# Kernel tuning notes

Measured on AMD Instinct MI355X. Metric: run time of the kernel, lower is better.

The kernel has to match this reference:

```python
import jax, jax.numpy as jnp
import numpy as np
import math

N, C, H = 2048, 256, 8
D = C // H
T, R, E = 8, 12, 32768
BUCKETS = 21
SEED = 128


def _layernorm(x, g, b, eps=1e-5):
    mu = jnp.mean(x, axis=-1, keepdims=True)
    var = jnp.var(x, axis=-1, keepdims=True)
    return (x - mu) * jax.lax.rsqrt(var + eps) * g + b


def _bucketize_dt(dt, num_buckets):
    eps = 1e-06
    signed_log = jnp.sign(dt) * jnp.log1p(jnp.abs(dt) + eps)
    min_v, max_v = -5.0, 5.0
    norm = (jnp.clip(signed_log, min_v, max_v) - min_v) / (max_v - min_v + 1e-09)
    idx = jnp.floor(norm * (num_buckets - 1)).astype(jnp.int32)
    return jnp.clip(idx, 0, num_buckets - 1)


def setup_inputs() -> dict:
    key = jax.random.key(0)
    ks = jax.random.split(key, 24)
    s = 0.02
    inp = {
        'X': jax.random.normal(ks[0], (N, C), jnp.float32),
        'token_type': jax.random.randint(ks[1], (N,), 0, T, jnp.int32),
        'edge_src': jax.random.randint(ks[2], (E,), 0, N, jnp.int32),
        'edge_dst': jax.random.randint(ks[3], (E,), 0, N, jnp.int32),
        'edge_rel': jax.random.randint(ks[4], (E,), 0, R, jnp.int32),
        'time_vec': jax.random.normal(ks[5], (N,), jnp.float32),
        'seed_count': SEED,
        'Wq': jax.random.normal(ks[6], (C, C), jnp.float32) * s,
        'bq': jnp.zeros((C,), jnp.float32),
        'Wk': jax.random.normal(ks[7], (C, C), jnp.float32) * s,
        'bk': jnp.zeros((C,), jnp.float32),
        'Wv': jax.random.normal(ks[8], (C, C), jnp.float32) * s,
        'bv': jnp.zeros((C,), jnp.float32),
        'Wo': jax.random.normal(ks[9], (C, C), jnp.float32) * s,
        'bo': jnp.zeros((C,), jnp.float32),
        'ln1_g': jnp.ones((C,), jnp.float32),
        'ln1_b': jnp.zeros((C,), jnp.float32),
        'ln2_g': jnp.ones((C,), jnp.float32),
        'ln2_b': jnp.zeros((C,), jnp.float32),
        'W1': jax.random.normal(ks[10], (C, 4 * C), jnp.float32) * s,
        'b1': jnp.zeros((4 * C,), jnp.float32),
        'W2': jax.random.normal(ks[11], (4 * C, C), jnp.float32) * s,
        'b2': jnp.zeros((C,), jnp.float32),
        'adj_rel_bias': jnp.zeros((R, H), jnp.float32),
        'typepair_bias': jnp.zeros((T, T, H), jnp.float32),
        'temp_bias': jax.random.normal(ks[12], (BUCKETS, H), jnp.float32) * s,
    }
    return inp


def reference(X, token_type, edge_src, edge_dst, edge_rel, time_vec, seed_count,
              Wq, bq, Wk, bk, Wv, bv, Wo, bo,
              ln1_g, ln1_b, ln2_g, ln2_b, W1, b1, W2, b2,
              adj_rel_bias, typepair_bias, temp_bias):
    n = X.shape[0]
    h = _layernorm(X, ln1_g, ln1_b)
    q = (h @ Wq + bq).reshape(n, H, D)
    k = (h @ Wk + bk).reshape(n, H, D)
    v = (h @ Wv + bv).reshape(n, H, D)
    scores = jnp.einsum('nhd,mhd->hnm', q, k) / math.sqrt(D)  # [H, N, N]

    # structural bias, factored as [N, N, H] then transposed
    bias = typepair_bias[token_type][:, token_type]            # [N, N, H]
    bias = bias.at[edge_src, edge_dst].add(adj_rel_bias[edge_rel])
    # seed-wise temporal bias on the first seed_count rows
    dt = time_vec[None, :] - time_vec[:seed_count, None]       # [S, N]
    tb = temp_bias[_bucketize_dt(dt, BUCKETS)]                 # [S, N, H]
    bias = bias.at[:seed_count].add(tb)

    attn = jax.nn.softmax(scores + bias.transpose(2, 0, 1), axis=-1)
    o = jnp.einsum('hnm,mhd->nhd', attn, v).reshape(n, C)
    x = X + (o @ Wo + bo)

    h2 = _layernorm(x, ln2_g, ln2_b)
    f = jax.nn.gelu(h2 @ W1 + b1, approximate=False) @ W2 + b2
    return x + f
```

## Files before the change

### kernel.cpp

```cpp
#include <hip/hip_runtime.h>
#include <hip/hip_bf16.h>
#include <math.h>

#define NTOK 2048
#define CDIM 256
#define HHEADS 8
#define DHEAD 32
#define NEDGE 32768
#define NTILE2 32
#define EXTD 64
#define LE 72
#define LP2 136

typedef __attribute__((ext_vector_type(8))) short short8;
typedef __attribute__((ext_vector_type(4))) short short4v;
typedef __attribute__((ext_vector_type(4))) float f32x4;

static __device__ inline short f2bf(float f) {
    __hip_bfloat16 h = __float2bfloat16(f);
    return *reinterpret_cast<short*>(&h);
}
static __device__ inline float bf2f(short s) {
    unsigned int u = ((unsigned int)(unsigned short)s) << 16;
    return *reinterpret_cast<float*>(&u);
}

static __device__ inline void transpose_tile_f32(const float* __restrict__ in,
    short* __restrict__ out, int K, int N, int k0, int n0, int t)
{
    __shared__ float tile[64][65];
    int r0 = t >> 4, c0 = (t & 15) * 4;
    #pragma unroll
    for (int i = 0; i < 4; i++) {
        int r = r0 + i * 16;
        float4 v = *(const float4*)(in + (size_t)(k0 + r) * N + n0 + c0);
        tile[r][c0 + 0] = v.x; tile[r][c0 + 1] = v.y;
        tile[r][c0 + 2] = v.z; tile[r][c0 + 3] = v.w;
    }
    __syncthreads();
    #pragma unroll
    for (int i = 0; i < 4; i++) {
        int nr = r0 + i * 16;
        short o4[4];
        #pragma unroll
        for (int j = 0; j < 4; j++) o4[j] = f2bf(tile[c0 + j][nr]);
        *(short4v*)(out + (size_t)(n0 + nr) * K + k0 + c0) = *(short4v*)o4;
    }
}

__global__ __launch_bounds__(256) void prep_kernel(
    const float* __restrict__ Wq, const float* __restrict__ Wk,
    const float* __restrict__ Wv, const float* __restrict__ Wo,
    const float* __restrict__ W1, const float* __restrict__ W2,
    short* __restrict__ wt_qkv, short* __restrict__ wot,
    short* __restrict__ w1t, short* __restrict__ w2t,
    const int* __restrict__ token_type, const float* __restrict__ typepair_bias,
    short* __restrict__ qh, short* __restrict__ kh,
    int* __restrict__ cnt2, float* __restrict__ rowsum,
    const float* __restrict__ X, const float* __restrict__ ln1_g,
    const float* __restrict__ ln1_b, short* __restrict__ h1)
{
    int b = blockIdx.x;
    int t = threadIdx.x;
    if (b < 192) {
        const float* src; short* dst; int K, N, bx, by;
        if (b < 64) {
            int m = b >> 4, r = b & 15;
            src = (m == 0) ? Wq : (m == 1) ? Wk : (m == 2) ? Wv : Wo;
            dst = (m == 0) ? wt_qkv : (m == 1) ? wt_qkv + 256 * 256
                : (m == 2) ? wt_qkv + 512 * 256 : wot;
            K = 256; N = 256; bx = r & 3; by = r >> 2;
        } else if (b < 128) {
            int r = b - 64; src = W1; dst = w1t; K = 256; N = 1024; bx = r & 15; by = r >> 4;
        } else {
            int r = b - 128; src = W2; dst = w2t; K = 1024; N = 256; bx = r & 3; by = r >> 2;
        }
        transpose_tile_f32(src, dst, K, N, by * 64, bx * 64, t);
    } else if (b < 256) {
        int idx = (b - 192) * 256 + t;
        int row = idx >> 3, h = idx & 7;
        int tt = token_type[row];
        short qe[32], ke[32];
        #pragma unroll
        for (int j = 0; j < 32; j++) {
            if (j < 8) {
                qe[j] = f2bf(typepair_bias[(tt * 8 + j) * 8 + h]);
                ke[j] = (j == tt) ? (short)0x3F80 : (short)0;
            } else { qe[j] = 0; ke[j] = 0; }
        }
        size_t base = ((size_t)h * NTOK + row) * EXTD + 32;
        #pragma unroll
        for (int k = 0; k < 4; k++) {
            *(short8*)&qh[base + k * 8] = *(short8*)&qe[k * 8];
            *(short8*)&kh[base + k * 8] = *(short8*)&ke[k * 8];
        }
    } else if (b < 288) {
        int base = (b - 256) * 2048 + t * 8;
        #pragma unroll
        for (int i = 0; i < 8; i++) cnt2[base + i] = 0;
    } else if (b < 296) {
        int base = (b - 288) * 2048 + t * 8;
        #pragma unroll
        for (int i = 0; i < 8; i++) rowsum[base + i] = 0.0f;
    } else {
        int wv = t >> 6, lane = t & 63;
        int row = (b - 296) * 4 + wv;
        float4 x = *(const float4*)&X[(size_t)row * CDIM + lane * 4];
        float s = x.x + x.y + x.z + x.w;
        #pragma unroll
        for (int off = 1; off < 64; off <<= 1) s += __shfl_xor(s, off);
        float mu = s * (1.0f / CDIM);
        float4 d = { x.x - mu, x.y - mu, x.z - mu, x.w - mu };
        float s2 = d.x * d.x + d.y * d.y + d.z * d.z + d.w * d.w;
        #pragma unroll
        for (int off = 1; off < 64; off <<= 1) s2 += __shfl_xor(s2, off);
        float rsig = rsqrtf(s2 * (1.0f / CDIM) + 1e-5f);
        float4 gg = *(const float4*)&ln1_g[lane * 4];
        float4 bb = *(const float4*)&ln1_b[lane * 4];
        short o4[4];
        o4[0] = f2bf(d.x * rsig * gg.x + bb.x);
        o4[1] = f2bf(d.y * rsig * gg.y + bb.y);
        o4[2] = f2bf(d.z * rsig * gg.z + bb.z);
        o4[3] = f2bf(d.w * rsig * gg.w + bb.w);
        *(short4v*)&h1[(size_t)row * CDIM + lane * 4] = *(short4v*)o4;
    }
}

__global__ __launch_bounds__(256) void ln4_kernel(const float* __restrict__ X,
    const float* __restrict__ g, const float* __restrict__ b, short* __restrict__ out)
{
    int t = threadIdx.x;
    int wv = t >> 6, lane = t & 63;
    int row = blockIdx.x * 4 + wv;

    float4 x = *(const float4*)&X[(size_t)row * CDIM + lane * 4];
    float s = x.x + x.y + x.z + x.w;
    #pragma unroll
    for (int off = 1; off < 64; off <<= 1) s += __shfl_xor(s, off);
    float mu = s * (1.0f / CDIM);
    float4 d = { x.x - mu, x.y - mu, x.z - mu, x.w - mu };
    float s2 = d.x * d.x + d.y * d.y + d.z * d.z + d.w * d.w;
    #pragma unroll
    for (int off = 1; off < 64; off <<= 1) s2 += __shfl_xor(s2, off);
    float rsig = rsqrtf(s2 * (1.0f / CDIM) + 1e-5f);
    float4 gg = *(const float4*)&g[lane * 4];
    float4 bb = *(const float4*)&b[lane * 4];
    short o4[4];
    o4[0] = f2bf(d.x * rsig * gg.x + bb.x);
    o4[1] = f2bf(d.y * rsig * gg.y + bb.y);
    o4[2] = f2bf(d.z * rsig * gg.z + bb.z);
    o4[3] = f2bf(d.w * rsig * gg.w + bb.w);
    *(short4v*)&out[(size_t)row * CDIM + lane * 4] = *(short4v*)o4;
}

template<int EPI>
__global__ __launch_bounds__(256) void gemm32_kernel(
    const short* __restrict__ A, const short* __restrict__ Bt,
    const float* __restrict__ bias, const float* __restrict__ resid,
    void* __restrict__ out_, int M, int N, int K)
{
    __shared__ short A_lds[32 * 40];
    __shared__ short B_lds[64 * 40];

    const int t = threadIdx.x;
    const int w = t >> 6, lane = t & 63, c = lane & 15, g = lane >> 4;
    const int row0 = blockIdx.y * 32, col0 = blockIdx.x * 64;
    const int srow = t >> 2, sk = (t & 3) * 8;

    f32x4 acc[2] = {};

    for (int k0 = 0; k0 < K; k0 += 32) {
        if (t < 128)
            *(short8*)&A_lds[srow * 40 + sk] = *(const short8*)&A[(size_t)(row0 + srow) * K + k0 + sk];
        *(short8*)&B_lds[srow * 40 + sk] = *(const short8*)&Bt[(size_t)(col0 + srow) * K + k0 + sk];
        __syncthreads();
        short8 af = *(const short8*)&A_lds[((w & 1) * 16 + c) * 40 + g * 8];
        #pragma unroll
        for (int nf = 0; nf < 2; nf++) {
            short8 bf = *(const short8*)&B_lds[((w >> 1) * 32 + nf * 16 + c) * 40 + g * 8];
            acc[nf] = __builtin_amdgcn_mfma_f32_16x16x32_bf16(af, bf, acc[nf], 0, 0, 0);
        }
        __syncthreads();
    }

    #pragma unroll
    for (int nf = 0; nf < 2; nf++) {
        #pragma unroll
        for (int reg = 0; reg < 4; reg++) {
            int row = row0 + (w & 1) * 16 + g * 4 + reg;
            int col = col0 + (w >> 1) * 32 + nf * 16 + c;
            float v = acc[nf][reg] + bias[col];
            if (EPI == 2) {
                ((float*)out_)[(size_t)row * N + col] = v + resid[(size_t)row * N + col];
            } else {
                v = 0.5f * v * (1.0f + erff(v * 0.70710678118654752f));
                ((short*)out_)[(size_t)row * N + col] = f2bf(v);
            }
        }
    }
}

__global__ __launch_bounds__(256) void gemm32_qkv_kernel(
    const short* __restrict__ A, const short* __restrict__ Bt,
    const float* __restrict__ bq, const float* __restrict__ bk, const float* __restrict__ bv,
    short* __restrict__ qh, short* __restrict__ kh, short* __restrict__ vt)
{
    const int K = CDIM;
    __shared__ short A_lds[32 * 40];
    __shared__ short B_lds[64 * 40];

    const int t = threadIdx.x;
    const int w = t >> 6, lane = t & 63, c = lane & 15, g = lane >> 4;
    const int row0 = blockIdx.y * 32, col0 = blockIdx.x * 64;
    const int srow = t >> 2, sk = (t & 3) * 8;

    f32x4 acc[2] = {};

    for (int k0 = 0; k0 < K; k0 += 32) {
        if (t < 128)
            *(short8*)&A_lds[srow * 40 + sk] = *(const short8*)&A[(size_t)(row0 + srow) * K + k0 + sk];
        *(short8*)&B_lds[srow * 40 + sk] = *(const short8*)&Bt[(size_t)(col0 + srow) * K + k0 + sk];
        __syncthreads();
        short8 af = *(const short8*)&A_lds[((w & 1) * 16 + c) * 40 + g * 8];
        #pragma unroll
        for (int nf = 0; nf < 2; nf++) {
            short8 bf = *(const short8*)&B_lds[((w >> 1) * 32 + nf * 16 + c) * 40 + g * 8];
            acc[nf] = __builtin_amdgcn_mfma_f32_16x16x32_bf16(af, bf, acc[nf], 0, 0, 0);
        }
        __syncthreads();
    }

    const int region = col0 >> 8;
    const int colr0 = col0 & 255;
    const float* bias = (region == 0) ? bq : (region == 1) ? bk : bv;
    #pragma unroll
    for (int nf = 0; nf < 2; nf++) {
        #pragma unroll
        for (int reg = 0; reg < 4; reg++) {
            int row = row0 + (w & 1) * 16 + g * 4 + reg;
            int col = colr0 + (w >> 1) * 32 + nf * 16 + c;
            float v = acc[nf][reg] + bias[col];
            if (region == 0) v *= 0.17677669529663687f;
            short bb = f2bf(v);
            size_t hidx = ((size_t)(col >> 5) * NTOK + row) * EXTD + (col & 31);
            if (region == 0)      qh[hidx] = bb;
            else if (region == 1) kh[hidx] = bb;
            else {
                int rl = row & 63;
                int rp = ((rl & 15) << 2) | (rl >> 4);
                vt[(size_t)col * NTOK + (row & ~63) + rp] = bb;
            }
        }
    }
}

__global__ void edge_hist2_kernel(const int* __restrict__ src, const int* __restrict__ dst,
    int* __restrict__ cnt, int E)
{
    int e = blockIdx.x * blockDim.x + threadIdx.x;
    if (e < E) atomicAdd(&cnt[src[e] * NTILE2 + (dst[e] >> 6)], 1);
}

__global__ __launch_bounds__(256) void edge_scan2_kernel(const int* __restrict__ cnt,
    int* __restrict__ row_ptr, int* __restrict__ wcur)
{
    __shared__ int sums[256];
    int t = threadIdx.x;
    int base = t * 256;
    int s = 0;
    for (int i = 0; i < 64; i++) {
        int4 v = *(const int4*)&cnt[base + i * 4];
        s += v.x + v.y + v.z + v.w;
    }
    sums[t] = s;
    __syncthreads();
    for (int off = 1; off < 256; off <<= 1) {
        int v = (t >= off) ? sums[t - off] : 0;
        __syncthreads();
        sums[t] += v;
        __syncthreads();
    }
    int run = (t == 0) ? 0 : sums[t - 1];
    for (int i = 0; i < 64; i++) {
        int4 v = *(const int4*)&cnt[base + i * 4];
        int4 o;
        o.x = run; run += v.x;
        o.y = run; run += v.y;
        o.z = run; run += v.z;
        o.w = run; run += v.w;
        *(int4*)&row_ptr[base + i * 4] = o;
        *(int4*)&wcur[base + i * 4] = o;
    }
    if (t == 255) row_ptr[NTOK * NTILE2] = run;
}

__global__ void edge_scatter2_kernel(const int* __restrict__ src, const int* __restrict__ dst,
    const int* __restrict__ rel, int* __restrict__ wcur, int2* __restrict__ pairs, int E)
{
    int e = blockIdx.x * blockDim.x + threadIdx.x;
    if (e < E) {
        int d = dst[e];
        int pos = atomicAdd(&wcur[src[e] * NTILE2 + (d >> 6)], 1);
        pairs[pos] = make_int2(d, rel[e]);
    }
}

__global__ __launch_bounds__(256) void sgemm_exp_kernel(
    const short* __restrict__ qh, const short* __restrict__ kh,
    const float* __restrict__ time_vec, const int* __restrict__ seed_ptr,
    const float* __restrict__ adj_rel_bias, const float* __restrict__ temp_bias,
    const int* __restrict__ row_ptr2, const int2* __restrict__ pairs2,
    short* __restrict__ S, float* __restrict__ rowsum)
{
    __shared__ short A_lds[64 * LE];
    __shared__ short B_lds[64 * LE];
    __shared__ float tcol_s[64];
    __shared__ float temp_h[21];
    __shared__ float adj_h[12];
    __shared__ int rpA[64], rpB[64];

    const int t = threadIdx.x;
    const int w = t >> 6, lane = t & 63, c = lane & 15, g = lane >> 4;
    const int h = blockIdx.z;
    const int m0 = blockIdx.x * 64, n0 = blockIdx.y * 64;
    const int seed = seed_ptr[0];

    {
        int r = t >> 3, off = (t & 7) * 8;
        *(short8*)&A_lds[r * LE + off] =
            *(const short8*)&qh[((size_t)h * NTOK + n0 + r) * EXTD + off];
        *(short8*)&A_lds[(r + 32) * LE + off] =
            *(const short8*)&qh[((size_t)h * NTOK + n0 + 32 + r) * EXTD + off];
        *(short8*)&B_lds[r * LE + off] =
            *(const short8*)&kh[((size_t)h * NTOK + m0 + r) * EXTD + off];
        *(short8*)&B_lds[(r + 32) * LE + off] =
            *(const short8*)&kh[((size_t)h * NTOK + m0 + 32 + r) * EXTD + off];
    }
    if (t < 64) {
        tcol_s[t] = time_vec[m0 + t];
        int bidx = (n0 + t) * NTILE2 + (m0 >> 6);
        rpA[t] = row_ptr2[bidx];
        rpB[t] = row_ptr2[bidx + 1];
    }
    if (t < 21) temp_h[t] = temp_bias[t * HHEADS + h];
    if (t < 12) adj_h[t] = adj_rel_bias[t * HHEADS + h];
    __syncthreads();

    short8 alo = *(const short8*)&A_lds[(w * 16 + c) * LE + g * 8];
    short8 ahi = *(const short8*)&A_lds[(w * 16 + c) * LE + 32 + g * 8];
    f32x4 acc[4] = {};
    #pragma unroll
    for (int nf = 0; nf < 4; nf++) {
        short8 blo = *(const short8*)&B_lds[(nf * 16 + c) * LE + g * 8];
        short8 bhi = *(const short8*)&B_lds[(nf * 16 + c) * LE + 32 + g * 8];
        acc[nf] = __builtin_amdgcn_mfma_f32_16x16x32_bf16(alo, blo, acc[nf], 0, 0, 0);
        acc[nf] = __builtin_amdgcn_mfma_f32_16x16x32_bf16(ahi, bhi, acc[nf], 0, 0, 0);
    }

    #pragma unroll
    for (int reg = 0; reg < 4; reg++) {
        const int rloc = w * 16 + g * 4 + reg;
        const int n = n0 + rloc;
        const bool rowTemp = (n < seed);
        const float tn = rowTemp ? time_vec[n] : 0.0f;

        {
            int e0 = rpA[rloc], e1 = rpB[rloc];
            for (int e = e0; e < e1; ++e) {
                int2 pr = pairs2[e];
                int cl = pr.x & 63;
                if ((cl & 15) == c) {
                    float ab = adj_h[pr.y];
                    int nfi = cl >> 4;
                    #pragma unroll
                    for (int nf = 0; nf < 4; nf++)
                        if (nf == nfi) acc[nf][reg] += ab;
                }
            }
        }

        float rsum = 0.0f;
        short p4[4];
        #pragma unroll
        for (int nf = 0; nf < 4; nf++) {
            float s = acc[nf][reg];
            if (rowTemp) {
                float dt = tcol_s[nf * 16 + c] - tn;
                float ab = fabsf(dt) + 1e-6f;
                float sg = (dt > 0.0f) ? 1.0f : ((dt < 0.0f) ? -1.0f : 0.0f);
                float sl = sg * log1pf(ab);
                sl = fminf(fmaxf(sl, -5.0f), 5.0f);
                float norm = (sl + 5.0f) * (1.0f / (10.0f + 1e-9f));
                int bidx = (int)floorf(norm * 20.0f);
                bidx = min(max(bidx, 0), 20);
                s += temp_h[bidx];
            }
            float e = __expf(s);
            rsum += e;
            p4[nf] = f2bf(e);
        }
        *(short4v*)&S[((size_t)h * NTOK + n) * NTOK + m0 + c * 4] = *(short4v*)p4;
        rsum += __shfl_xor(rsum, 1);
        rsum += __shfl_xor(rsum, 2);
        rsum += __shfl_xor(rsum, 4);
        rsum += __shfl_xor(rsum, 8);
        if (c == 0) atomicAdd(&rowsum[h * NTOK + n], rsum);
    }
}

__global__ __launch_bounds__(256) void pv_kernel(
    const short* __restrict__ P, const short* __restrict__ vt,
    const float* __restrict__ rowsum, short* __restrict__ o)
{
    __shared__ short A_lds[32 * LP2];
    __shared__ short B_lds[32 * LP2];
    const int t = threadIdx.x;
    const int w = t >> 6, lane = t & 63, c = lane & 15, g = lane >> 4;
    const int h = blockIdx.y;
    const int n0 = blockIdx.x * 32;
    const int rowblk = (w & 1) * 16, colblk = (w >> 1) * 16;

    f32x4 acc = {0.0f, 0.0f, 0.0f, 0.0f};

    for (int k0 = 0; k0 < NTOK; k0 += 128) {
        #pragma unroll
        for (int i = 0; i < 2; i++) {
            int s = t + i * 256;
            int r = s >> 4, off = (s & 15) * 8;
            *(short8*)&A_lds[r * LP2 + off] =
                *(const short8*)&P[((size_t)h * NTOK + n0 + r) * NTOK + k0 + off];
            *(short8*)&B_lds[r * LP2 + off] =
                *(const short8*)&vt[(size_t)(h * 32 + r) * NTOK + k0 + off];
        }
        __syncthreads();
        #pragma unroll
        for (int kk = 0; kk < 4; kk++) {
            short8 af = *(const short8*)&A_lds[(rowblk + c) * LP2 + kk * 32 + g * 8];
            short8 bf = *(const short8*)&B_lds[(colblk + c) * LP2 + kk * 32 + g * 8];
            acc = __builtin_amdgcn_mfma_f32_16x16x32_bf16(af, bf, acc, 0, 0, 0);
        }
        __syncthreads();
    }

    #pragma unroll
    for (int reg = 0; reg < 4; reg++) {
        int row = n0 + rowblk + g * 4 + reg;
        int col = h * 32 + colblk + c;
        float inv = 1.0f / rowsum[h * NTOK + row];
        o[(size_t)row * CDIM + col] = f2bf(acc[reg] * inv);
    }
}

extern "C" void kernel_launch(void* const* d_in, const int* in_sizes, int n_in,
                              void* d_out, int out_size, void* d_ws, size_t ws_size,
                              hipStream_t stream)
{
    (void)in_sizes; (void)n_in; (void)out_size; (void)ws_size;
    const float* X        = (const float*)d_in[0];
    const int* token_type = (const int*)d_in[1];
    const int* edge_src   = (const int*)d_in[2];
    const int* edge_dst   = (const int*)d_in[3];
    const int* edge_rel   = (const int*)d_in[4];
    const float* time_vec = (const float*)d_in[5];
    const int* seed_ptr   = (const int*)d_in[6];
    const float* Wq = (const float*)d_in[7];  const float* bq = (const float*)d_in[8];
    const float* Wk = (const float*)d_in[9];  const float* bk = (const float*)d_in[10];
    const float* Wv = (const float*)d_in[11]; const float* bv = (const float*)d_in[12];
    const float* Wo = (const float*)d_in[13]; const float* bo = (const float*)d_in[14];
    const float* ln1_g = (const float*)d_in[15]; const float* ln1_b = (const float*)d_in[16];
    const float* ln2_g = (const float*)d_in[17]; const float* ln2_b = (const float*)d_in[18];
    const float* W1 = (const float*)d_in[19]; const float* b1 = (const float*)d_in[20];
    const float* W2 = (const float*)d_in[21]; const float* b2 = (const float*)d_in[22];
    const float* adj_rel_bias  = (const float*)d_in[23];
    const float* typepair_bias = (const float*)d_in[24];
    const float* temp_bias     = (const float*)d_in[25];
    float* out = (float*)d_out;

    char* base = (char*)d_ws;
    size_t off = 0;
    auto alloc = [&](size_t bytes) { char* p = base + off; off += (bytes + 255) & ~(size_t)255; return p; };
    short* qh_bf   = (short*)alloc((size_t)HHEADS * NTOK * EXTD * 2);
    short* kh_bf   = (short*)alloc((size_t)HHEADS * NTOK * EXTD * 2);
    short* vt_bf   = (short*)alloc((size_t)256 * NTOK * 2);
    short* h1_bf   = (short*)alloc((size_t)NTOK * 256 * 2);
    short* h2_bf   = (short*)alloc((size_t)NTOK * 256 * 2);
    short* o_bf    = (short*)alloc((size_t)NTOK * 256 * 2);
    short* mid_bf  = (short*)alloc((size_t)NTOK * 1024 * 2);
    float* xb      = (float*)alloc((size_t)NTOK * 256 * 4);
    short* wt_qkv  = (short*)alloc((size_t)768 * 256 * 2);
    short* wot     = (short*)alloc((size_t)256 * 256 * 2);
    short* w1t     = (short*)alloc((size_t)1024 * 256 * 2);
    short* w2t     = (short*)alloc((size_t)256 * 1024 * 2);
    int2*  pairs2  = (int2*)alloc((size_t)NEDGE * 8);
    int*   cnt2    = (int*)alloc((size_t)NTOK * NTILE2 * 4);
    int*   rowptr2 = (int*)alloc(((size_t)NTOK * NTILE2 + 4) * 4);
    int*   wcur2   = (int*)alloc((size_t)NTOK * NTILE2 * 4);
    float* rowsum  = (float*)alloc((size_t)HHEADS * NTOK * 4);
    short* S       = (short*)alloc((size_t)HHEADS * NTOK * NTOK * 2);

    prep_kernel<<<808, 256, 0, stream>>>(Wq, Wk, Wv, Wo, W1, W2,
                                         wt_qkv, wot, w1t, w2t,
                                         token_type, typepair_bias,
                                         qh_bf, kh_bf, cnt2, rowsum,
                                         X, ln1_g, ln1_b, h1_bf);

    edge_hist2_kernel<<<NEDGE / 256, 256, 0, stream>>>(edge_src, edge_dst, cnt2, NEDGE);
    edge_scan2_kernel<<<1, 256, 0, stream>>>(cnt2, rowptr2, wcur2);
    edge_scatter2_kernel<<<NEDGE / 256, 256, 0, stream>>>(edge_src, edge_dst, edge_rel, wcur2, pairs2, NEDGE);

    gemm32_qkv_kernel<<<dim3(12, 64), 256, 0, stream>>>(h1_bf, wt_qkv, bq, bk, bv,
                                                        qh_bf, kh_bf, vt_bf);

    sgemm_exp_kernel<<<dim3(32, 32, 8), 256, 0, stream>>>(
        qh_bf, kh_bf, time_vec, seed_ptr, adj_rel_bias, temp_bias,
        rowptr2, pairs2, S, rowsum);
    pv_kernel<<<dim3(64, 8), 256, 0, stream>>>(S, vt_bf, rowsum, o_bf);

    gemm32_kernel<2><<<dim3(4, 64), 256, 0, stream>>>(o_bf, wot, bo, X, xb, NTOK, 256, 256);

    ln4_kernel<<<NTOK / 4, 256, 0, stream>>>(xb, ln2_g, ln2_b, h2_bf);

    gemm32_kernel<3><<<dim3(16, 64), 256, 0, stream>>>(h2_bf, w1t, b1, nullptr, mid_bf, NTOK, 1024, 256);
    gemm32_kernel<2><<<dim3(4, 64), 256, 0, stream>>>(mid_bf, w2t, b2, xb, out, NTOK, 256, 1024);
}
```

Before: 149.8 us.

## Store attention probabilities and V in fp8 and use fp8 MFMA for PV

New measurement: 146.0 us. 1.03x faster.

```diff
diff --git a/kernel.cpp b/kernel.cpp
--- a/kernel.cpp
+++ b/kernel.cpp
@@ -10,7 +10,7 @@
 #define NTILE2 32
 #define EXTD 64
 #define LE 72
-#define LP2 136
+#define LP3 144
 
 typedef __attribute__((ext_vector_type(8))) short short8;
 typedef __attribute__((ext_vector_type(4))) short short4v;
@@ -23,6 +23,10 @@
 static __device__ inline float bf2f(short s) {
     unsigned int u = ((unsigned int)(unsigned short)s) << 16;
     return *reinterpret_cast<float*>(&u);
+}
+static __device__ inline unsigned char f2fp8(float f) {
+    int pk = __builtin_amdgcn_cvt_pk_fp8_f32(f, f, 0, false);
+    return (unsigned char)(pk & 0xFF);
 }
 
 static __device__ inline void transpose_tile_f32(const float* __restrict__ in,
@@ -203,7 +207,7 @@
 __global__ __launch_bounds__(256) void gemm32_qkv_kernel(
     const short* __restrict__ A, const short* __restrict__ Bt,
     const float* __restrict__ bq, const float* __restrict__ bk, const float* __restrict__ bv,
-    short* __restrict__ qh, short* __restrict__ kh, short* __restrict__ vt)
+    short* __restrict__ qh, short* __restrict__ kh, unsigned char* __restrict__ vt8)
 {
     const int K = CDIM;
     __shared__ short A_lds[32 * 40];
@@ -241,14 +245,15 @@
             int col = colr0 + (w >> 1) * 32 + nf * 16 + c;
             float v = acc[nf][reg] + bias[col];
             if (region == 0) v *= 0.17677669529663687f;
-            short bb = f2bf(v);
-            size_t hidx = ((size_t)(col >> 5) * NTOK + row) * EXTD + (col & 31);
-            if (region == 0)      qh[hidx] = bb;
-            else if (region == 1) kh[hidx] = bb;
-            else {
+            if (region < 2) {
+                short bb = f2bf(v);
+                size_t hidx = ((size_t)(col >> 5) * NTOK + row) * EXTD + (col & 31);
+                if (region == 0) qh[hidx] = bb;
+                else             kh[hidx] = bb;
+            } else {
                 int rl = row & 63;
                 int rp = ((rl & 15) << 2) | (rl >> 4);
-                vt[(size_t)col * NTOK + (row & ~63) + rp] = bb;
+                vt8[(size_t)col * NTOK + (row & ~63) + rp] = f2fp8(v);
             }
         }
     }
@@ -310,7 +315,7 @@
     const float* __restrict__ time_vec, const int* __restrict__ seed_ptr,
     const float* __restrict__ adj_rel_bias, const float* __restrict__ temp_bias,
     const int* __restrict__ row_ptr2, const int2* __restrict__ pairs2,
-    short* __restrict__ S, float* __restrict__ rowsum)
+    unsigned char* __restrict__ S8, float* __restrict__ rowsum)
 {
     __shared__ short A_lds[64 * LE];
     __shared__ short B_lds[64 * LE];
@@ -380,7 +385,7 @@
         }
 
         float rsum = 0.0f;
-        short p4[4];
+        float ev[4];
         #pragma unroll
         for (int nf = 0; nf < 4; nf++) {
             float s = acc[nf][reg];
@@ -397,9 +402,12 @@
             }
             float e = __expf(s);
             rsum += e;
-            p4[nf] = f2bf(e);
-        }
-        *(short4v*)&S[((size_t)h * NTOK + n) * NTOK + m0 + c * 4] = *(short4v*)p4;
+            ev[nf] = e;
+        }
+        int lo = __builtin_amdgcn_cvt_pk_fp8_f32(ev[0], ev[1], 0, false);
+        int hi = __builtin_amdgcn_cvt_pk_fp8_f32(ev[2], ev[3], 0, false);
+        unsigned word = ((unsigned)lo & 0xFFFFu) | ((unsigned)hi << 16);
+        *(unsigned*)&S8[((size_t)h * NTOK + n) * NTOK + m0 + c * 4] = word;
         rsum += __shfl_xor(rsum, 1);
         rsum += __shfl_xor(rsum, 2);
         rsum += __shfl_xor(rsum, 4);
@@ -409,11 +417,11 @@
 }
 
 __global__ __launch_bounds__(256) void pv_kernel(
-    const short* __restrict__ P, const short* __restrict__ vt,
+    const unsigned char* __restrict__ P8, const unsigned char* __restrict__ vt8,
     const float* __restrict__ rowsum, short* __restrict__ o)
 {
-    __shared__ short A_lds[32 * LP2];
-    __shared__ short B_lds[32 * LP2];
+    __shared__ __align__(16) unsigned char A_lds[32 * LP3];
+    __shared__ __align__(16) unsigned char B_lds[32 * LP3];
     const int t = threadIdx.x;
     const int w = t >> 6, lane = t & 63, c = lane & 15, g = lane >> 4;
     const int h = blockIdx.y;
@@ -423,21 +431,17 @@
     f32x4 acc = {0.0f, 0.0f, 0.0f, 0.0f};
 
     for (int k0 = 0; k0 < NTOK; k0 += 128) {
-        #pragma unroll
-        for (int i = 0; i < 2; i++) {
-            int s = t + i * 256;
-            int r = s >> 4, off = (s & 15) * 8;
-            *(short8*)&A_lds[r * LP2 + off] =
-                *(const short8*)&P[((size_t)h * NTOK + n0 + r) * NTOK + k0 + off];
-            *(short8*)&B_lds[r * LP2 + off] =
-                *(const short8*)&vt[(size_t)(h * 32 + r) * NTOK + k0 + off];
-        }
+        int r = t >> 3, off = (t & 7) * 16;
+        *(int4*)&A_lds[r * LP3 + off] =
+            *(const int4*)&P8[((size_t)h * NTOK + n0 + r) * NTOK + k0 + off];
+        *(int4*)&B_lds[r * LP3 + off] =
+            *(const int4*)&vt8[(size_t)(h * 32 + r) * NTOK + k0 + off];
         __syncthreads();
         #pragma unroll
         for (int kk = 0; kk < 4; kk++) {
-            short8 af = *(const short8*)&A_lds[(rowblk + c) * LP2 + kk * 32 + g * 8];
-            short8 bf = *(const short8*)&B_lds[(colblk + c) * LP2 + kk * 32 + g * 8];
-            acc = __builtin_amdgcn_mfma_f32_16x16x32_bf16(af, bf, acc, 0, 0, 0);
+            long long a = *(const long long*)&A_lds[(rowblk + c) * LP3 + kk * 32 + g * 8];
+            long long b = *(const long long*)&B_lds[(colblk + c) * LP3 + kk * 32 + g * 8];
+            acc = __builtin_amdgcn_mfma_f32_16x16x32_fp8_fp8(a, b, acc, 0, 0, 0);
         }
         __syncthreads();
     }
@@ -481,7 +485,7 @@
     auto alloc = [&](size_t bytes) { char* p = base + off; off += (bytes + 255) & ~(size_t)255; return p; };
     short* qh_bf   = (short*)alloc((size_t)HHEADS * NTOK * EXTD * 2);
     short* kh_bf   = (short*)alloc((size_t)HHEADS * NTOK * EXTD * 2);
-    short* vt_bf   = (short*)alloc((size_t)256 * NTOK * 2);
+    unsigned char* vt8 = (unsigned char*)alloc((size_t)256 * NTOK);
     short* h1_bf   = (short*)alloc((size_t)NTOK * 256 * 2);
     short* h2_bf   = (short*)alloc((size_t)NTOK * 256 * 2);
     short* o_bf    = (short*)alloc((size_t)NTOK * 256 * 2);
@@ -496,7 +500,7 @@
     int*   rowptr2 = (int*)alloc(((size_t)NTOK * NTILE2 + 4) * 4);
     int*   wcur2   = (int*)alloc((size_t)NTOK * NTILE2 * 4);
     float* rowsum  = (float*)alloc((size_t)HHEADS * NTOK * 4);
-    short* S       = (short*)alloc((size_t)HHEADS * NTOK * NTOK * 2);
+    unsigned char* S8 = (unsigned char*)alloc((size_t)HHEADS * NTOK * NTOK);
 
     prep_kernel<<<808, 256, 0, stream>>>(Wq, Wk, Wv, Wo, W1, W2,
                                          wt_qkv, wot, w1t, w2t,
@@ -509,12 +513,12 @@
     edge_scatter2_kernel<<<NEDGE / 256, 256, 0, stream>>>(edge_src, edge_dst, edge_rel, wcur2, pairs2, NEDGE);
 
     gemm32_qkv_kernel<<<dim3(12, 64), 256, 0, stream>>>(h1_bf, wt_qkv, bq, bk, bv,
-                                                        qh_bf, kh_bf, vt_bf);
+                                                        qh_bf, kh_bf, vt8);
 
     sgemm_exp_kernel<<<dim3(32, 32, 8), 256, 0, stream>>>(
         qh_bf, kh_bf, time_vec, seed_ptr, adj_rel_bias, temp_bias,
-        rowptr2, pairs2, S, rowsum);
-    pv_kernel<<<dim3(64, 8), 256, 0, stream>>>(S, vt_bf, rowsum, o_bf);
+        rowptr2, pairs2, S8, rowsum);
+    pv_kernel<<<dim3(64, 8), 256, 0, stream>>>(S8, vt8, rowsum, o_bf);
 
     gemm32_kernel<2><<<dim3(4, 64), 256, 0, stream>>>(o_bf, wot, bo, X, xb, NTOK, 256, 256);
 
```
